# Kernel optimization log

Hardware: AMD Instinct MI355X
Metric: run time of the kernel (lower is better)

## Reference

```python
import jax, jax.numpy as jnp
import numpy as np

N, M, K, R, D = 2048, 64, 2, 512, 1024   # seq len, chunk size, neighbours, neighbour len, model dim
H, L = 16, 1024                           # heads, layer_size
LCH = N // M                              # number of chunks l = 32
DH = L // H
SCALE = 1.0 / (D ** 0.5)                  # source scales by input dim, not head dim


def setup_inputs() -> dict:
    key = jax.random.key(0)
    ks = jax.random.split(key, 6)
    s = 0.02
    return {
        "x": jax.random.normal(ks[0], (N, D), jnp.float32),
        "neighbours": jax.random.normal(ks[1], (LCH, K, R, D), jnp.float32),
        "Wq": jax.random.normal(ks[2], (L, D), jnp.float32) * s,
        "Wk": jax.random.normal(ks[3], (L, D), jnp.float32) * s,
        "Wv": jax.random.normal(ks[4], (L, D), jnp.float32) * s,
        "Wo": jax.random.normal(ks[5], (D, L), jnp.float32) * s,
    }


def _attend(q_in, ctx, Wq, Wk, Wv, Wo):
    # q_in: (B, Q, D) queries; ctx: (B, K, R, D) retrieved neighbours.
    # Batches the per-chunk, per-neighbour Attention calls of the source in one pass,
    # then means over the K neighbour axis (reduce 'k m d -> m d', 'mean').
    B, Q = q_in.shape[0], q_in.shape[1]
    q = (q_in @ Wq.T).reshape(B, Q, H, DH)                     # (B,Q,H,DH)
    kk = (ctx @ Wk.T).reshape(B, K, R, H, DH)                  # (B,K,R,H,DH)
    vv = (ctx @ Wv.T).reshape(B, K, R, H, DH)
    scores = jnp.einsum('bqhe,bkrhe->bkhrq', q, kk) * SCALE    # (B,K,H,R,Q)
    # FAITHFUL quirk: source softmaxes over the QUERY axis (last dim of 'b k q')
    w = jax.nn.softmax(scores, axis=-1)
    o = jnp.einsum('bkhrq,bkrhe->bkqhe', w, vv).reshape(B, K, Q, L)
    z = jnp.einsum('bkql,dl->bkqd', o, Wo)                     # output projection (dropout=0)
    return z.mean(axis=1)                                      # mean over neighbours -> (B,Q,D)


def reference(x, neighbours, Wq, Wk, Wv, Wo):
    # attending_chunks: shift input left by m-1, zero-pad bottom, chunk into (l, m, d)
    att = jnp.concatenate([x[M - 1:], jnp.zeros((M - 1, D), x.dtype)], axis=0).reshape(LCH, M, D)
    # main loop over chunks u in [0, l-2] and their k neighbours, fully batched
    main = _attend(att[:LCH - 1], neighbours[:LCH - 1], Wq, Wk, Wv, Wo)   # (l-1, M, D)
    # last token attends to neighbours[-1]
    last = _attend(x[-1][None, None, :], neighbours[-1][None], Wq, Wk, Wv, Wo)  # (1,1,D)
    body = jnp.concatenate([main.reshape(-1, D), att[-1]], axis=0)        # (N, D)
    # pad top with m-1 zeros, keep first n rows
    out = jnp.concatenate([jnp.zeros((M - 1, D), x.dtype), body[:N - M + 1]], axis=0)
    out = out.at[:M - 1].set(x[:M - 1])
    out = out.at[-1].set(last[0, 0])
    return out
```

## Files before the change

### kernel.cpp

```cpp
#include <hip/hip_runtime.h>
#include <hip/hip_bf16.h>


using u16 = unsigned short;
using u32 = unsigned int;

typedef float  f32x4   __attribute__((ext_vector_type(4)));
typedef __bf16 bf16x8v __attribute__((ext_vector_type(8)));
typedef __bf16 bf16x4v __attribute__((ext_vector_type(4)));
typedef short  s16x4   __attribute__((ext_vector_type(4)));
typedef u16    u16x8   __attribute__((ext_vector_type(8)));
typedef u16    u16x4v  __attribute__((ext_vector_type(4)));

#define SCALE_LOG2E (1.4426950408889634f / 32.0f)

__device__ __forceinline__ u16 f2b(float f){ return __builtin_bit_cast(u16, (__bf16)f); }
__device__ __forceinline__ int swz(int row, int cb){ return row*128 + (cb ^ ((row & 7) << 4)); }

__device__ __forceinline__ void gl_lds16(const void* g, void* l) {
    __builtin_amdgcn_global_load_lds(
        (const __attribute__((address_space(1))) unsigned int*)(unsigned long long)g,
        (__attribute__((address_space(3))) unsigned int*)(unsigned int)(unsigned long long)l,
        16, 0, 0);
}

template<bool AF32, int OM>
__global__ __launch_bounds__(256)
void gemm128(const void* __restrict__ Ap, int lda,
             const u16* __restrict__ Bp, int ldb,
             void* __restrict__ Cp, void* __restrict__ Cp2,
             int M, int Kc, int row_off, int nNt)
{
    __shared__ char As[128*128];
    __shared__ char Bs[128*128];
    const int tid  = threadIdx.x;
    const int lane = tid & 63, wave = tid >> 6;
    const int li = lane & 15, lg = lane >> 4;
    const int wr = wave >> 1, wc = wave & 1;

    const int nwg  = gridDim.x;
    const int lin  = blockIdx.x;
    const int lin2 = (lin & 7) * (nwg >> 3) + (lin >> 3);
    const long bm = (long)(lin2 / nNt) * 128;
    const long bn = (long)(lin2 % nNt) * 128;

    const int grow = wave*32 + (lane >> 3);
    const int gcol = ((lane & 7) ^ (lane >> 3)) << 3;
    const int sr = tid >> 1, sc = (tid & 1) * 32;
    long arow_f = bm + sr; if (arow_f >= M) arow_f = M - 1;
    long arow_g[4];
    #pragma unroll
    for (int j = 0; j < 4; j++) {
        long r = bm + grow + j*8;
        arow_g[j] = (r < M) ? r : (M - 1);
    }

    f32x4 acc[4][4] = {};

    for (int k0 = 0; k0 < Kc; k0 += 64) {
        float4 a4[8];
        if (AF32) {
            const float4* ap = (const float4*)((const float*)Ap + arow_f*lda + k0 + sc);
            #pragma unroll
            for (int i = 0; i < 8; i++) a4[i] = ap[i];
        }
        __syncthreads();
        if (!AF32) {
            #pragma unroll
            for (int j = 0; j < 4; j++)
                gl_lds16((const u16*)Ap + arow_g[j]*(long)lda + k0 + gcol,
                         As + (wave*4 + j)*1024);
        }
        #pragma unroll
        for (int j = 0; j < 4; j++)
            gl_lds16(Bp + (bn + grow + j*8)*(long)ldb + k0 + gcol,
                     Bs + (wave*4 + j)*1024);
        if (AF32) {
            #pragma unroll
            for (int i = 0; i < 4; i++) {
                float4 f0 = a4[2*i], f1 = a4[2*i+1];
                bf16x8v w;
                w[0]=(__bf16)f0.x; w[1]=(__bf16)f0.y; w[2]=(__bf16)f0.z; w[3]=(__bf16)f0.w;
                w[4]=(__bf16)f1.x; w[5]=(__bf16)f1.y; w[6]=(__bf16)f1.z; w[7]=(__bf16)f1.w;
                *(bf16x8v*)(As + swz(sr, sc*2 + i*16)) = w;
            }
        }
        __syncthreads();
        #pragma unroll
        for (int es = 0; es < 2; es++) {
            bf16x8v af[4], bfv[4];
            #pragma unroll
            for (int mt = 0; mt < 4; mt++)
                af[mt] = *(const bf16x8v*)(As + swz(wr*64 + mt*16 + li, es*64 + lg*16));
            #pragma unroll
            for (int nt = 0; nt < 4; nt++)
                bfv[nt] = *(const bf16x8v*)(Bs + swz(wc*64 + nt*16 + li, es*64 + lg*16));
            #pragma unroll
            for (int mt = 0; mt < 4; mt++)
                #pragma unroll
                for (int nt = 0; nt < 4; nt++)
                    acc[mt][nt] = __builtin_amdgcn_mfma_f32_16x16x32_bf16(
                        af[mt], bfv[nt], acc[mt][nt], 0, 0, 0);
        }
    }

    #pragma unroll
    for (int mt = 0; mt < 4; mt++) {
        #pragma unroll
        for (int nt = 0; nt < 4; nt++) {
            f32x4 c = acc[mt][nt];
            const long row0 = bm + wr*64 + mt*16 + lg*4;
            const long col  = bn + wc*64 + nt*16 + li;
            if (OM == 0) {
                u16* C = (u16*)Cp;
                #pragma unroll
                for (int j = 0; j < 4; j++) {
                    long rg = row0 + j;
                    if (rg < M) C[rg*1024 + col] = f2b(c[j]);
                }
            } else if (OM == 2) {
                float* C = (float*)Cp;
                #pragma unroll
                for (int j = 0; j < 4; j++) {
                    long rg = row0 + j;
                    if (rg < M) C[(row_off + rg)*1024 + col] = c[j];
                }
            } else {
                if (col < 1024) {
                    u16* Ka = (u16*)Cp;
                    #pragma unroll
                    for (int j = 0; j < 4; j++) Ka[(row0 + j)*1024 + col] = f2b(c[j]);
                } else {
                    u16* Vt = (u16*)Cp2;
                    bf16x4v w;
                    #pragma unroll
                    for (int j = 0; j < 4; j++) w[j] = (__bf16)c[j];
                    *(bf16x4v*)(Vt + (col - 1024)*32768L + row0) = w;
                }
            }
        }
    }
}

__global__ __launch_bounds__(256)
void attn_kernel(const u16* __restrict__ Qa, const u16* __restrict__ Ka,
                 const u16* __restrict__ Vt, u16* __restrict__ Om)
{
    const int u = blockIdx.x, h = blockIdx.y;
    const int tid = threadIdx.x;
    const int lane = tid & 63, wave = tid >> 6;
    const int li = lane & 15, lg = lane >> 4;

    bf16x8v qf[4][2];
    #pragma unroll
    for (int qt = 0; qt < 4; qt++)
        #pragma unroll
        for (int es = 0; es < 2; es++)
            qf[qt][es] = *(const bf16x8v*)(Qa + (long)(63 + u*64 + qt*16 + li)*1024
                                              + h*64 + es*32 + lg*8);

    f32x4 acc[4][4] = {};

    for (int it = wave; it < 64; it += 4) {
        const int k = it >> 5, rsub = it & 31;
        const long kr = (long)u*1024 + k*512 + rsub*16;

        bf16x8v a0 = *(const bf16x8v*)(Ka + (kr + li)*1024 + h*64 + lg*8);
        bf16x8v a1 = *(const bf16x8v*)(Ka + (kr + li)*1024 + h*64 + 32 + lg*8);
        f32x4 s[4];
        #pragma unroll
        for (int qt = 0; qt < 4; qt++) {
            f32x4 c = {};
            c = __builtin_amdgcn_mfma_f32_16x16x32_bf16(a0, qf[qt][0], c, 0, 0, 0);
            c = __builtin_amdgcn_mfma_f32_16x16x32_bf16(a1, qf[qt][1], c, 0, 0, 0);
            s[qt] = c;
        }
        float p[4][4];
        #pragma unroll
        for (int qt = 0; qt < 4; qt++)
            #pragma unroll
            for (int j = 0; j < 4; j++)
                p[qt][j] = __builtin_amdgcn_exp2f(s[qt][j]);
        float rz[4];
        #pragma unroll
        for (int j = 0; j < 4; j++) {
            float z = p[0][j] + p[1][j] + p[2][j] + p[3][j];
            z += __shfl_xor(z, 1); z += __shfl_xor(z, 2);
            z += __shfl_xor(z, 4); z += __shfl_xor(z, 8);
            rz[j] = __builtin_amdgcn_rcpf(z);
        }
        s16x4 wf[4];
        #pragma unroll
        for (int qt = 0; qt < 4; qt++) {
            bf16x4v w;
            #pragma unroll
            for (int j = 0; j < 4; j++) w[j] = (__bf16)(p[qt][j] * rz[j]);
            wf[qt] = __builtin_bit_cast(s16x4, w);
        }
        #pragma unroll
        for (int et = 0; et < 4; et++) {
            s16x4 va = *(const s16x4*)(Vt + (long)(h*64 + et*16 + li)*32768 + kr + lg*4);
            #pragma unroll
            for (int qt = 0; qt < 4; qt++)
                acc[et][qt] = __builtin_amdgcn_mfma_f32_16x16x16bf16_1k(
                    va, wf[qt], acc[et][qt], 0, 0, 0);
        }
    }

    __shared__ float Osum[64*64];
    for (int w = 0; w < 4; w++) {
        if (wave == w) {
            #pragma unroll
            for (int et = 0; et < 4; et++)
                #pragma unroll
                for (int qt = 0; qt < 4; qt++)
                    #pragma unroll
                    for (int j = 0; j < 4; j++) {
                        int e = et*16 + lg*4 + j, q = qt*16 + li;
                        if (w == 0) Osum[e*64 + q]  = acc[et][qt][j];
                        else        Osum[e*64 + q] += acc[et][qt][j];
                    }
        }
        __syncthreads();
    }
    const int q = tid & 63, e0 = (tid >> 6) * 16;
    u16x8 o0, o1;
    #pragma unroll
    for (int i = 0; i < 8; i++) {
        o0[i] = f2b(0.5f * Osum[(e0 + i    )*64 + q]);
        o1[i] = f2b(0.5f * Osum[(e0 + 8 + i)*64 + q]);
    }
    u16* dst = Om + (long)(u*64 + q)*1024 + h*64 + e0;
    *(u16x8*)dst       = o0;
    *(u16x8*)(dst + 8) = o1;
}

__global__ __launch_bounds__(256)
void convert_w(const float* __restrict__ Wq, const float* __restrict__ Wk,
               const float* __restrict__ Wv, const float* __restrict__ Wo,
               u16* __restrict__ dst)
{
    int idx = blockIdx.x*256 + threadIdx.x;
    int w   = idx >> 18;
    int off = (idx & 262143) << 2;
    const float* src = (w == 0) ? Wq : (w == 1) ? Wk : (w == 2) ? Wv : Wo;
    float scv = (w == 0) ? SCALE_LOG2E : 1.0f;
    float4 v = *(const float4*)(src + off);
    u16x4v o = { f2b(v.x*scv), f2b(v.y*scv), f2b(v.z*scv), f2b(v.w*scv) };
    *(u16x4v*)(dst + (long)w*1048576 + off) = o;
}

__global__ __launch_bounds__(256)
void convert_a(const float* __restrict__ src, u16* __restrict__ dst, int n8)
{
    int i = blockIdx.x*256 + threadIdx.x;
    const int stride = gridDim.x*256;
    for (; i < n8; i += stride) {
        float4 f0 = ((const float4*)src)[2*i], f1 = ((const float4*)src)[2*i+1];
        u16x8 o = { f2b(f0.x), f2b(f0.y), f2b(f0.z), f2b(f0.w),
                    f2b(f1.x), f2b(f1.y), f2b(f1.z), f2b(f1.w) };
        ((u16x8*)dst)[i] = o;
    }
}

__global__ __launch_bounds__(256)
void last_kernel(const u16* __restrict__ Vt, u16* __restrict__ Om)
{
    const int row  = blockIdx.x*4 + (threadIdx.x >> 6);
    const int lane = threadIdx.x & 63;
    const u16* p = Vt + (long)row*32768 + 31*1024 + lane*16;
    float s = 0.f;
    #pragma unroll
    for (int hf = 0; hf < 2; hf++) {
        bf16x8v v = *(const bf16x8v*)(p + hf*8);
        #pragma unroll
        for (int i = 0; i < 8; i++) s += (float)v[i];
    }
    #pragma unroll
    for (int m = 1; m < 64; m <<= 1) s += __shfl_xor(s, m);
    if (lane == 0) Om[(long)1984*1024 + row] = f2b(0.5f * s);
}

__global__ __launch_bounds__(256)
void copy_head(const float* __restrict__ x, float* __restrict__ out)
{
    int i = blockIdx.x*256 + threadIdx.x;
    ((float4*)out)[i] = ((const float4*)x)[i];
}

extern "C" void kernel_launch(void* const* d_in, const int* in_sizes, int n_in,
                              void* d_out, int out_size, void* d_ws, size_t ws_size,
                              hipStream_t stream)
{
    const float* x  = (const float*)d_in[0];
    const float* nb = (const float*)d_in[1];
    const float* Wq = (const float*)d_in[2];
    const float* Wk = (const float*)d_in[3];
    const float* Wv = (const float*)d_in[4];
    const float* Wo = (const float*)d_in[5];
    float* out = (float*)d_out;
    char*  ws  = (char*)d_ws;

    if (ws_size < (size_t)144*1024*1024) return;
    const bool big = ws_size >= (size_t)212*1024*1024;
    u16* wW  = (u16*)ws;
    u16* Qa  = (u16*)(ws + (size_t) 8*1024*1024);
    u16* Om  = (u16*)(ws + (size_t)12*1024*1024);
    u16* Ka  = (u16*)(ws + (size_t)16*1024*1024);
    u16* Vt  = (u16*)(ws + (size_t)80*1024*1024);
    u16* Anb = (u16*)(ws + (size_t)144*1024*1024);
    u16* xb  = (u16*)(ws + (size_t)208*1024*1024);
    u16* wWq = wW, *wWk = wW + 1048576, *wWo = wW + 3*1048576;

    convert_w<<<dim3(4096), dim3(256), 0, stream>>>(Wq, Wk, Wv, Wo, wW);

    if (big) {
        convert_a<<<dim3(2048), dim3(256), 0, stream>>>(nb, Anb, 4194304);
        convert_a<<<dim3(512),  dim3(256), 0, stream>>>(x,  xb,  262144);
        gemm128<false, 0><<<dim3(128), dim3(256), 0, stream>>>(
            xb, 1024, wWq, 1024, Qa, nullptr, 2048, 1024, 0, 8);
        gemm128<false, 3><<<dim3(4096), dim3(256), 0, stream>>>(
            Anb, 1024, wWk, 1024, Ka, Vt, 32768, 1024, 0, 16);
    } else {
        gemm128<true, 0><<<dim3(128), dim3(256), 0, stream>>>(
            x, 1024, wWq, 1024, Qa, nullptr, 2048, 1024, 0, 8);
        gemm128<true, 3><<<dim3(4096), dim3(256), 0, stream>>>(
            nb, 1024, wWk, 1024, Ka, Vt, 32768, 1024, 0, 16);
    }

    attn_kernel<<<dim3(31, 16), dim3(256), 0, stream>>>(Qa, Ka, Vt, Om);
    last_kernel<<<dim3(256),    dim3(256), 0, stream>>>(Vt, Om);

    gemm128<false, 2><<<dim3(128), dim3(256), 0, stream>>>(
        Om, 1024, wWo, 1024, out, nullptr, 1985, 1024, 63, 8);
    copy_head<<<dim3(63), dim3(256), 0, stream>>>(x, out);
}
```

Baseline: 289.0 us.

## Use 256x256-tile 512-thread GEMM with interleaved staging for K/V projection

Adds a new gemm256 kernel with 256x256 output tiles, 8 waves and 128KB LDS double buffering. It interleaves global-to-LDS loads of the next K-slice with MFMA quarter-steps under barriers and raises MFMA priority. It replaces the 128-tile GEMM for the large neighbour K/V projection on the big-workspace path. The aim is higher arithmetic intensity and better overlap of memory and compute. The cost is more LDS per block, more registers and only two blocks per CU.

```diff
diff --git a/kernel.cpp b/kernel.cpp
--- a/kernel.cpp
+++ b/kernel.cpp
@@ -22,6 +22,156 @@
         (const __attribute__((address_space(1))) unsigned int*)(unsigned long long)g,
         (__attribute__((address_space(3))) unsigned int*)(unsigned int)(unsigned long long)l,
         16, 0, 0);
+}
+
+template<int OM>
+__global__ __launch_bounds__(512, 2)
+void gemm256(const u16* __restrict__ Ap, int lda,
+             const u16* __restrict__ Bp, int ldb,
+             void* __restrict__ Cp, void* __restrict__ Cp2,
+             int M, int Kc, int nNt)
+{
+    __shared__ char Ls[131072];
+    char* const Abase = Ls;
+    char* const Bbase = Ls + 65536;
+
+    const int tid  = threadIdx.x;
+    const int lane = tid & 63, wave = tid >> 6;
+    const int li = lane & 15, lg = lane >> 4;
+    const int wr = wave >> 2, wc = wave & 3;
+
+    const int nwg  = gridDim.x;
+    const int lin  = blockIdx.x;
+    const int lin2 = (lin & 7) * (nwg >> 3) + (lin >> 3);
+    const long bm = (long)(lin2 / nNt) * 256;
+    const long bn = (long)(lin2 % nNt) * 256;
+
+    const int srow = tid >> 3;
+    const int scol = ((tid & 7) ^ (srow & 7)) << 3;
+
+    auto stageA = [&](int t, int hh) {
+        char* d = Abase + (t & 1)*32768 + hh*16384 + wave*1024;
+        long r0 = bm + hh*128 + srow;      if (r0 >= M) r0 = M - 1;
+        long r1 = bm + hh*128 + 64 + srow; if (r1 >= M) r1 = M - 1;
+        gl_lds16(Ap + r0*(long)lda + (long)t*64 + scol, d);
+        gl_lds16(Ap + r1*(long)lda + (long)t*64 + scol, d + 8192);
+    };
+    auto stageB = [&](int t, int hh) {
+        char* d = Bbase + (t & 1)*32768 + hh*16384 + wave*1024;
+        long r0 = bn + hh*128 + srow;
+        gl_lds16(Bp + r0*(long)ldb + (long)t*64 + scol, d);
+        gl_lds16(Bp + (r0 + 64)*(long)ldb + (long)t*64 + scol, d + 8192);
+    };
+
+    const int NT = Kc >> 6;
+
+    stageB(0, 0); stageB(0, 1); stageA(0, 0); stageA(0, 1); stageB(1, 0);
+    asm volatile("s_waitcnt vmcnt(2)" ::: "memory");
+    asm volatile("s_barrier" ::: "memory");
+
+    const int swx = (li & 7) << 4;
+    const int cb0 = (lg*16) ^ swx;
+    const int cb1 = (64 + lg*16) ^ swx;
+    const int arb = li;
+    const int brb = (wc & 1)*64 + li;
+
+    f32x4 acc[8][4] = {};
+    bf16x8v a[4], b[4];
+
+#define MFMA16(MH)                                                              \
+    __builtin_amdgcn_s_setprio(1);                                              \
+    _Pragma("unroll") for (int mt = 0; mt < 4; mt++)                            \
+        _Pragma("unroll") for (int nt = 0; nt < 4; nt++)                        \
+            acc[(MH)*4 + mt][nt] = __builtin_amdgcn_mfma_f32_16x16x32_bf16(     \
+                a[mt], b[nt], acc[(MH)*4 + mt][nt], 0, 0, 0);                   \
+    __builtin_amdgcn_s_setprio(0);
+
+#define BAR_IN()  asm volatile("s_barrier" ::: "memory");                       \
+                  asm volatile("s_waitcnt lgkmcnt(0)" ::: "memory");            \
+                  __builtin_amdgcn_sched_barrier(0);
+#define BAR_OUT() asm volatile("s_barrier" ::: "memory");
+
+    for (int t = 0; t < NT - 1; ++t) {
+        char* At = Abase + (t & 1)*32768 + wr*16384;
+        char* Bt = Bbase + (t & 1)*32768 + (wc >> 1)*16384;
+
+        #pragma unroll
+        for (int mt = 0; mt < 4; mt++) a[mt] = *(const bf16x8v*)(At + (arb + mt*16)*128 + cb0);
+        #pragma unroll
+        for (int nt = 0; nt < 4; nt++) b[nt] = *(const bf16x8v*)(Bt + (brb + nt*16)*128 + cb0);
+        stageB(t + 1, 1);
+        BAR_IN(); MFMA16(0); BAR_OUT();
+        #pragma unroll
+        for (int mt = 0; mt < 4; mt++) a[mt] = *(const bf16x8v*)(At + (arb + 64 + mt*16)*128 + cb0);
+        stageA(t + 1, 0);
+        BAR_IN(); MFMA16(1); BAR_OUT();
+        #pragma unroll
+        for (int mt = 0; mt < 4; mt++) a[mt] = *(const bf16x8v*)(At + (arb + mt*16)*128 + cb1);
+        #pragma unroll
+        for (int nt = 0; nt < 4; nt++) b[nt] = *(const bf16x8v*)(Bt + (brb + nt*16)*128 + cb1);
+        stageA(t + 1, 1);
+        BAR_IN(); MFMA16(0); BAR_OUT();
+        #pragma unroll
+        for (int mt = 0; mt < 4; mt++) a[mt] = *(const bf16x8v*)(At + (arb + 64 + mt*16)*128 + cb1);
+        if (t + 2 < NT) stageB(t + 2, 0);
+        BAR_IN(); MFMA16(1);
+        asm volatile("s_waitcnt vmcnt(2)" ::: "memory");
+        BAR_OUT();
+    }
+    {
+        const int t = NT - 1;
+        char* At = Abase + (t & 1)*32768 + wr*16384;
+        char* Bt = Bbase + (t & 1)*32768 + (wc >> 1)*16384;
+        asm volatile("s_waitcnt vmcnt(0)" ::: "memory");
+        asm volatile("s_barrier" ::: "memory");
+        #pragma unroll
+        for (int mt = 0; mt < 4; mt++) a[mt] = *(const bf16x8v*)(At + (arb + mt*16)*128 + cb0);
+        #pragma unroll
+        for (int nt = 0; nt < 4; nt++) b[nt] = *(const bf16x8v*)(Bt + (brb + nt*16)*128 + cb0);
+        BAR_IN(); MFMA16(0); BAR_OUT();
+        #pragma unroll
+        for (int mt = 0; mt < 4; mt++) a[mt] = *(const bf16x8v*)(At + (arb + 64 + mt*16)*128 + cb0);
+        BAR_IN(); MFMA16(1); BAR_OUT();
+        #pragma unroll
+        for (int mt = 0; mt < 4; mt++) a[mt] = *(const bf16x8v*)(At + (arb + mt*16)*128 + cb1);
+        #pragma unroll
+        for (int nt = 0; nt < 4; nt++) b[nt] = *(const bf16x8v*)(Bt + (brb + nt*16)*128 + cb1);
+        BAR_IN(); MFMA16(0); BAR_OUT();
+        #pragma unroll
+        for (int mt = 0; mt < 4; mt++) a[mt] = *(const bf16x8v*)(At + (arb + 64 + mt*16)*128 + cb1);
+        BAR_IN(); MFMA16(1); BAR_OUT();
+    }
+#undef MFMA16
+#undef BAR_IN
+#undef BAR_OUT
+
+    #pragma unroll
+    for (int ai = 0; ai < 8; ai++) {
+        #pragma unroll
+        for (int nt = 0; nt < 4; nt++) {
+            f32x4 c = acc[ai][nt];
+            const long row0 = bm + wr*128 + (ai >> 2)*64 + (ai & 3)*16 + lg*4;
+            const long col  = bn + wc*64 + nt*16 + li;
+            if (OM == 3) {
+                if (col < 1024) {
+                    u16* Ka = (u16*)Cp;
+                    #pragma unroll
+                    for (int j = 0; j < 4; j++) {
+                        long rg = row0 + j;
+                        if (rg < M) Ka[rg*1024 + col] = f2b(c[j]);
+                    }
+                } else {
+                    u16* Vt = (u16*)Cp2;
+                    if (row0 + 3 < M) {
+                        bf16x4v w;
+                        #pragma unroll
+                        for (int j = 0; j < 4; j++) w[j] = (__bf16)c[j];
+                        *(bf16x4v*)(Vt + (col - 1024)*32768L + row0) = w;
+                    }
+                }
+            }
+        }
+    }
 }
 
 template<bool AF32, int OM>
@@ -319,8 +469,8 @@
         convert_a<<<dim3(512),  dim3(256), 0, stream>>>(x,  xb,  262144);
         gemm128<false, 0><<<dim3(128), dim3(256), 0, stream>>>(
             xb, 1024, wWq, 1024, Qa, nullptr, 2048, 1024, 0, 8);
-        gemm128<false, 3><<<dim3(4096), dim3(256), 0, stream>>>(
-            Anb, 1024, wWk, 1024, Ka, Vt, 32768, 1024, 0, 16);
+        gemm256<3><<<dim3(1024), dim3(512), 0, stream>>>(
+            Anb, 1024, wWk, 1024, Ka, Vt, 32768, 1024, 8);
     } else {
         gemm128<true, 0><<<dim3(128), dim3(256), 0, stream>>>(
             x, 1024, wWq, 1024, Qa, nullptr, 2048, 1024, 0, 8);
```

Result: faster. 267.5 us (-7.4%).
